# Performance work log

Hardware: AMD Instinct MI355X
Metric: run time of the kernel (lower is better)

## Reference

```python
import jax, jax.numpy as jnp
import numpy as np

B, S, D = 2, 2048, 1024
H, DK, DV = 16, 64, 64
MASKED = True


def setup_inputs() -> dict:
    key = jax.random.key(0)
    ks = jax.random.split(key, 12)
    s = 0.02
    inp = {
        "Q": jax.random.normal(ks[0], (B, S, D), jnp.float32),
        "K": jax.random.normal(ks[1], (B, S, D), jnp.float32),
        "V": jax.random.normal(ks[2], (B, S, D), jnp.float32),
        "pad_mask": jax.random.randint(ks[3], (B, S), 0, 2, jnp.int32),
        "Wq": jax.random.normal(ks[4], (D, H * DK), jnp.float32) * s,
        "bq": jnp.zeros((H * DK,), jnp.float32),
        "Wk": jax.random.normal(ks[5], (D, H * DK), jnp.float32) * s,
        "bk": jnp.zeros((H * DK,), jnp.float32),
        "Wv": jax.random.normal(ks[6], (D, H * DV), jnp.float32) * s,
        "bv": jnp.zeros((H * DV,), jnp.float32),
        "Wo": jax.random.normal(ks[7], (H * DV, D), jnp.float32) * s,
        "bo": jnp.zeros((D,), jnp.float32),
    }
    return inp


def _split(x):
    # [B,S,H*d] -> [B,H,S,d]
    b, s, _ = x.shape
    return x.reshape(b, s, H, -1).transpose(0, 2, 1, 3)


def reference(Q, K, V, pad_mask, Wq, bq, Wk, bk, Wv, bv, Wo, bo):
    q = _split(Q @ Wq + bq)  # [B,H,S,DK]
    k = _split(K @ Wk + bk)  # [B,H,S,DK]
    v = _split(V @ Wv + bv)  # [B,H,S,DV]

    scores = jnp.einsum("bhqd,bhkd->bhqk", q, k) / np.sqrt(DK)
    mask = pad_mask[:, None, None, :].astype(jnp.float32)  # [B,1,1,S]
    if MASKED:
        causal = jnp.triu(jnp.ones((S, S), jnp.float32), k=1)[None, None]
        mask = ((mask + causal) > 0).astype(jnp.float32)
    scores = scores - 1e9 * mask

    attn = jax.nn.softmax(scores, axis=-1)
    out = jnp.einsum("bhqk,bhkd->bhqd", attn, v)  # [B,H,S,DV]
    out = out.transpose(0, 2, 1, 3).reshape(B, S, H * DV)
    return out @ Wo + bo
```

## Files before the change

kernel.cpp:

```cpp
#include <hip/hip_runtime.h>

typedef unsigned short u16;
typedef unsigned int u32;

typedef __attribute__((ext_vector_type(8))) short bfrag;
typedef __attribute__((ext_vector_type(4))) float f32x4;
typedef __attribute__((ext_vector_type(8))) u16 u16x8;
typedef __attribute__((ext_vector_type(4))) u16 u16x4;

constexpr int S = 2048;
constexpr int HN = 16;
constexpr float QSCALE = 0.18033688011112042f;
constexpr float NBIG   = -1.442695e9f;

__device__ __forceinline__ u16 f2b(float f) {
  u32 u = __builtin_bit_cast(u32, f);
  return (u16)((u + 0x7FFFu + ((u >> 16) & 1u)) >> 16);
}
__device__ __forceinline__ float b2f(u16 v) {
  u32 u = (u32)v << 16;
  return __builtin_bit_cast(float, u);
}
__device__ __forceinline__ u32 cvtpk(float lo, float hi) {
  u32 d;
  asm("v_cvt_pk_bf16_f32 %0, %1, %2" : "=v"(d) : "v"(lo), "v"(hi));
  return d;
}
__device__ __forceinline__ float fexp2(float x) { return __builtin_amdgcn_exp2f(x); }

__device__ __forceinline__ f32x4 mfma16(bfrag a, bfrag b, f32x4 c) {
  return __builtin_amdgcn_mfma_f32_16x16x32_bf16(a, b, c, 0, 0, 0);
}

__device__ __forceinline__ void gload_lds16(const void* g, void* l) {
  __builtin_amdgcn_global_load_lds(
      (const __attribute__((address_space(1))) u32*)g,
      (__attribute__((address_space(3))) u32*)l, 16, 0, 0);
}

__global__ __launch_bounds__(256) void wtrans_kernel(
    const float* __restrict__ W0, const float* __restrict__ W1,
    const float* __restrict__ W2, const float* __restrict__ W3,
    u16* __restrict__ ws)
{
  const float* W = blockIdx.z == 0 ? W0 : blockIdx.z == 1 ? W1 : blockIdx.z == 2 ? W2 : W3;
  const float sc = blockIdx.z == 0 ? QSCALE : 1.0f;
  u16* WT = ws + (size_t)blockIdx.z * (1u << 20);
  __shared__ u16 tile[64 * 65];
  const int t = threadIdx.x;
  const int k0 = blockIdx.y * 64, n0 = blockIdx.x * 64;
#pragma unroll
  for (int i = 0; i < 4; ++i) {
    int idx = i * 256 + t;
    int r = idx >> 4, c4 = (idx & 15) * 4;
    float4 v = *(const float4*)&W[(size_t)(k0 + r) * 1024 + n0 + c4];
    tile[r * 65 + c4 + 0] = f2b(v.x * sc);
    tile[r * 65 + c4 + 1] = f2b(v.y * sc);
    tile[r * 65 + c4 + 2] = f2b(v.z * sc);
    tile[r * 65 + c4 + 3] = f2b(v.w * sc);
  }
  __syncthreads();
#pragma unroll
  for (int i = 0; i < 2; ++i) {
    int idx = i * 256 + t;
    int n = idx >> 3, k8 = (idx & 7) * 8;
    u16x8 o;
#pragma unroll
    for (int j = 0; j < 8; ++j) o[j] = tile[(k8 + j) * 65 + n];
    *(u16x8*)&WT[(size_t)(n0 + n) * 1024 + k0 + k8] = o;
  }
}

__global__ __launch_bounds__(256) void pscan_kernel(
    const int* __restrict__ pad, u16* __restrict__ idxc, u16* __restrict__ posT,
    int* __restrict__ eqt, float* __restrict__ colsumg)
{
  __shared__ int wtot[4];
  __shared__ int cntS;
  const int b = blockIdx.x;
  const int t = threadIdx.x, lane = t & 63, w = t >> 6;
  for (int i = t; i < 1024; i += 256) colsumg[b * 1024 + i] = 0.f;
  int4 p0 = *(const int4*)&pad[b * 2048 + t * 8];
  int4 p1 = *(const int4*)&pad[b * 2048 + t * 8 + 4];
  int u[8] = {p0.x == 0, p0.y == 0, p0.z == 0, p0.w == 0,
              p1.x == 0, p1.y == 0, p1.z == 0, p1.w == 0};
  int ps[8], run = 0;
#pragma unroll
  for (int j = 0; j < 8; ++j) { run += u[j]; ps[j] = run; }
  int sc = run;
#pragma unroll
  for (int o = 1; o < 64; o <<= 1) {
    int v = __shfl_up(sc, o);
    if (lane >= o) sc += v;
  }
  if (lane == 63) wtot[w] = sc;
  __syncthreads();
  int base = 0;
#pragma unroll
  for (int i = 0; i < 4; ++i) if (i < w) base += wtot[i];
  int excl = base + sc - run;
#pragma unroll
  for (int j = 0; j < 8; ++j)
    if (u[j]) idxc[b * 2048 + excl + ps[j] - 1] = (u16)(t * 8 + j);
  if ((t & 7) == 7) eqt[b * 32 + (t >> 3)] = base + sc;
  if (t == 255) cntS = base + sc;
  __syncthreads();
  const int cnt = cntS;
#pragma unroll
  for (int j = 0; j < 8; ++j) {
    int e = t * 8 + j;
    int pv = u[j] ? (excl + ps[j] - 1) : (cnt + e - excl - ps[j]);
    posT[b * 2048 + e] = (u16)pv;
  }
  for (int j = cnt + t; j < 2048; j += 256) idxc[b * 2048 + j] = 0x7FFF;
}

__global__ __launch_bounds__(256) void cvt_kernel(
    const float* __restrict__ A0, const float* __restrict__ A1,
    const float* __restrict__ A2, const u16* __restrict__ posT,
    u16* __restrict__ outbase)
{
  const int z = blockIdx.y;
  const float* A = z == 0 ? A0 : z == 1 ? A1 : A2;
  u16* dst = outbase + (size_t)z * (4u << 20);
  const int t = threadIdx.x;
  const int row = blockIdx.x * 2 + (t >> 7);
  const int col = (t & 127) * 8;
  int drow = row;
  if (z == 1) {
    int b = row >> 11;
    int p = posT[row];
    if (p >= 2048 - ((b == 0) ? 0 : 0)) {  }
    drow = b * 2048 + p;
  }
  const float* src = &A[(size_t)row * 1024 + col];
  float4 v0 = *(const float4*)src;
  float4 v1 = *(const float4*)(src + 4);
  union { u32 w[4]; u16x8 v; } o;
  o.w[0] = cvtpk(v0.x, v0.y); o.w[1] = cvtpk(v0.z, v0.w);
  o.w[2] = cvtpk(v1.x, v1.y); o.w[3] = cvtpk(v1.z, v1.w);
  *(u16x8*)&dst[(size_t)drow * 1024 + col] = o.v;
}

__global__ __launch_bounds__(256) void vgather_kernel(
    const u16* __restrict__ vb, const u16* __restrict__ idxc, u16* __restrict__ vTc)
{
  __shared__ u16 tile[64 * 65];
  const int ti = blockIdx.x, bh = blockIdx.y, b = bh >> 4;
  const int t = threadIdx.x;
#pragma unroll
  for (int i = 0; i < 2; ++i) {
    int idx = i * 256 + t;
    int r = idx >> 3, c8 = (idx & 7) * 8;
    int o = idxc[b * 2048 + ti * 64 + r];
    u16x8 in = {};
    if (o != 0x7FFF) in = *(const u16x8*)&vb[((size_t)bh * 2048 + o) * 64 + c8];
#pragma unroll
    for (int j = 0; j < 8; ++j) tile[r * 65 + c8 + j] = in[j];
  }
  __syncthreads();
#pragma unroll
  for (int i = 0; i < 2; ++i) {
    int idx = i * 256 + t;
    int dv = idx >> 3, s8 = (idx & 7) * 8;
    u16x8 o_;
#pragma unroll
    for (int j = 0; j < 8; ++j) o_[j] = tile[(s8 + j) * 65 + dv];
    int a = s8 >> 5, bb = (s8 >> 4) & 1, cc = (s8 >> 3) & 1;
    int s0l = a * 32 + cc * 16 + bb * 4;
    int x = (dv & 7) << 3;
    u16x4 lo = {o_[0], o_[1], o_[2], o_[3]};
    u16x4 hi = {o_[4], o_[5], o_[6], o_[7]};
    size_t rowbase = ((size_t)bh * 64 + dv) * S + ti * 64;
    *(u16x4*)&vTc[rowbase + (s0l ^ x)] = lo;
    *(u16x4*)&vTc[rowbase + ((s0l + 8) ^ x)] = hi;
  }
}

template <int CMODE>
__device__ __forceinline__ void gemm_core(
    u16* As, u16* Bs,
    const u16* __restrict__ A, const u16* __restrict__ Bt,
    const float* __restrict__ bias, void* __restrict__ Cout,
    int N, int K, int bn, int bm, float bscale,
    int kswz, float* __restrict__ csum)
{
  const int tid = threadIdx.x;
  const int wid = tid >> 6, lane = tid & 63;
  const int g = lane >> 4, c = lane & 15;
  const int wr = wid >> 1, wc = wid & 1;

  f32x4 acc[4][2] = {};

  const int nkt = K >> 6;
  for (int kt = 0; kt < nkt; ++kt) {
#pragma unroll
    for (int p = 0; p < 4; ++p) {
      int off = (p * 4 + wid) * 1024 + (lane << 4);
      int row = off >> 7, colb = off & 127;
      gload_lds16(&A[(size_t)(bm * 128 + row) * K + kt * 64 +
                     ((colb ^ ((row & 7) << 4)) >> 1)],
                  (char*)As + (p * 4 + wid) * 1024);
    }
#pragma unroll
    for (int p = 0; p < 2; ++p) {
      int off = (p * 4 + wid) * 1024 + (lane << 4);
      int row = off >> 7, colb = off & 127;
      gload_lds16(&Bt[(size_t)(bn * 64 + row) * K + kt * 64 +
                      ((colb ^ ((row & 7) << 4)) >> 1)],
                  (char*)Bs + (p * 4 + wid) * 1024);
    }
    __syncthreads();

#pragma unroll
    for (int ks = 0; ks < 2; ++ks) {
      bfrag af[4], bf[2];
#pragma unroll
      for (int mi = 0; mi < 4; ++mi) {
        int row = wr * 64 + mi * 16 + c;
        af[mi] = *(const bfrag*)&As[row * 64 + ((ks * 32 + g * 8) ^ ((row & 7) << 3))];
      }
#pragma unroll
      for (int ni = 0; ni < 2; ++ni) {
        int row = wc * 32 + ni * 16 + c;
        bf[ni] = *(const bfrag*)&Bs[row * 64 + ((ks * 32 + g * 8) ^ ((row & 7) << 3))];
      }
#pragma unroll
      for (int mi = 0; mi < 4; ++mi)
#pragma unroll
        for (int ni = 0; ni < 2; ++ni)
          acc[mi][ni] = mfma16(af[mi], bf[ni], acc[mi][ni]);
    }
    __syncthreads();
  }

  float colacc[2] = {0.f, 0.f};
#pragma unroll
  for (int mi = 0; mi < 4; ++mi) {
#pragma unroll
    for (int ni = 0; ni < 2; ++ni) {
#pragma unroll
      for (int j = 0; j < 4; ++j) {
        int rowg = bm * 128 + wr * 64 + mi * 16 + g * 4 + j;
        int colg = bn * 64 + wc * 32 + ni * 16 + c;
        float val = fmaf(bias[colg], bscale, acc[mi][ni][j]);
        if (CMODE == 0) {
          int b = rowg >> 11, s = rowg & (S - 1);
          int h = colg >> 6, d = colg & 63;
          if (kswz) d ^= (s & 7) << 3;
          if (csum) colacc[ni] += val;
          ((u16*)Cout)[((size_t)((b * HN + h) * S + s)) * 64 + d] = f2b(val);
        } else {
          ((float*)Cout)[(size_t)rowg * N + colg] = val;
        }
      }
    }
  }
  if (CMODE == 0 && csum) {
#pragma unroll
    for (int ni = 0; ni < 2; ++ni) {
      float s_ = colacc[ni];
      s_ += __shfl_xor(s_, 16);
      s_ += __shfl_xor(s_, 32);
      if (lane < 16) {
        int colg = bn * 64 + wc * 32 + ni * 16 + c;
        int b = (bm * 128) >> 11;
        atomicAdd(&csum[b * 1024 + colg], s_);
      }
    }
  }
}

__global__ __launch_bounds__(256) void qkv_gemm(
    const u16* __restrict__ Abase, const u16* __restrict__ WTbase,
    const float* __restrict__ b0, const float* __restrict__ b1, const float* __restrict__ b2,
    u16* __restrict__ qb, u16* __restrict__ kc, u16* __restrict__ vb,
    const int* __restrict__ eqt, float* __restrict__ colsumg)
{
  __shared__ __align__(16) u16 As[128 * 64];
  __shared__ __align__(16) u16 Bs[64 * 64];
  const int bid = blockIdx.x;
  const int l = (bid & 7) * 192 + (bid >> 3);
  const int z = l >> 9, rem = l & 511, bm = rem >> 4, bn = rem & 15;
  if (z == 1) {
    int b_ = (bm * 128) >> 11;
    int cnt_ = eqt[b_ * 32 + 31];
    if (((bm * 128) & 2047) >= cnt_) return;
  }
  const u16* A = Abase + (size_t)z * (4u << 20);
  const u16* Bt = WTbase + (size_t)z * (1u << 20);
  const float* bias = z == 0 ? b0 : z == 1 ? b1 : b2;
  u16* C = z == 0 ? qb : z == 1 ? kc : vb;
  gemm_core<0>(As, Bs, A, Bt, bias, C, 1024, 1024, bn, bm,
               z == 0 ? QSCALE : 1.0f,
               z == 1 ? 1 : 0,
               z == 2 ? colsumg : nullptr);
}

__global__ __launch_bounds__(256) void out_gemm(
    const u16* __restrict__ Av, const u16* __restrict__ Bt,
    const float* __restrict__ bias, void* __restrict__ Cout)
{
  __shared__ __align__(16) u16 As[128 * 64];
  __shared__ __align__(16) u16 Bs[64 * 64];
  const int bid = blockIdx.x;
  const int l = (bid & 7) * 64 + (bid >> 3);
  const int bm = l >> 4, bn = l & 15;
  gemm_core<1>(As, Bs, Av, Bt, bias, Cout, 1024, 1024, bn, bm, 1.0f,
               0, nullptr);
}

__global__ __launch_bounds__(256) void attn_kernel(
    const u16* __restrict__ q, const u16* __restrict__ kc,
    const u16* __restrict__ vTc, const u16* __restrict__ idxc,
    const int* __restrict__ eqt, const float* __restrict__ colsumg,
    u16* __restrict__ ao)
{
  __shared__ __align__(16) u16 Ks[2][64 * 64];
  __shared__ __align__(16) u16 Vs[2][64 * 64];

  const int tid = threadIdx.x;
  const int wid = tid >> 6, lane = tid & 63;
  const int g = lane >> 4, c = lane & 15;
  const int i = blockIdx.x;
  const int qt = 31 - (i >> 5);
  const int bh = i & 31;
  const int b = bh >> 4, h = bh & 15;

  const u16* idxb = idxc + b * 2048;
  const int ecnt = eqt[b * 32 + qt];
  const int nt = (ecnt + 63) >> 6;
  const int fz = idxb[0];
  const int qbasew = qt * 64 + wid * 16;
  const int qrow = qbasew + c;

  bfrag qf[2];
#pragma unroll
  for (int ks = 0; ks < 2; ++ks)
    qf[ks] = *(const bfrag*)&q[((size_t)bh * S + qrow) * 64 + ks * 32 + g * 8];

  float m = -3.0e38f, lsum = 0.f;
  f32x4 acc[4] = {};

  const size_t kbase = (size_t)bh * S * 64;
  const size_t vbase = (size_t)bh * 64 * S;
  const int sb = wid * 2048 + (lane << 4);
  const int sb2 = sb + 1024;

#define STAGE(buf, t)                                                              \
  do {                                                                             \
    gload_lds16(&kc[kbase + (size_t)(t) * 4096 + (sb >> 1)],                       \
                (char*)Ks[buf] + wid * 2048);                                      \
    gload_lds16(&kc[kbase + (size_t)(t) * 4096 + (sb2 >> 1)],                      \
                (char*)Ks[buf] + wid * 2048 + 1024);                               \
    gload_lds16(&vTc[vbase + (size_t)(sb >> 7) * S + (t) * 64 + ((sb & 127) >> 1)],\
                (char*)Vs[buf] + wid * 2048);                                      \
    gload_lds16(&vTc[vbase + (size_t)(sb2 >> 7) * S + (t) * 64 + ((sb2 & 127) >> 1)],\
                (char*)Vs[buf] + wid * 2048 + 1024);                               \
  } while (0)

  if (nt > 0) {
    STAGE(0, 0);
    __syncthreads();

    int cur = 0;
    for (int t = 0; t < nt; ++t) {
      if (t + 1 < nt) { STAGE(cur ^ 1, t + 1); }

      f32x4 sc[4] = {};
      __builtin_amdgcn_s_setprio(1);
#pragma unroll
      for (int ks = 0; ks < 2; ++ks)
#pragma unroll
        for (int nf = 0; nf < 4; ++nf) {
          int row = nf * 16 + c;
          bfrag kf = *(const bfrag*)&Ks[cur][row * 64 + ((ks * 32 + g * 8) ^ ((row & 7) << 3))];
          sc[nf] = mfma16(kf, qf[ks], sc[nf]);
        }
      __builtin_amdgcn_s_setprio(0);

      float sval[4][4];
#pragma unroll
      for (int nf = 0; nf < 4; ++nf)
#pragma unroll
        for (int r = 0; r < 4; ++r) sval[nf][r] = sc[nf][r];

      if ((int)idxb[t * 64 + 63] > qbasew) {
#pragma unroll
        for (int nf = 0; nf < 4; ++nf)
#pragma unroll
          for (int r = 0; r < 4; ++r) {
            int ov = idxb[t * 64 + nf * 16 + g * 4 + r];
            if (ov > qrow) sval[nf][r] = NBIG;
          }
      }

      float pm = sval[0][0];
#pragma unroll
      for (int nf = 0; nf < 4; ++nf)
#pragma unroll
        for (int r = 0; r < 4; ++r) pm = fmaxf(pm, sval[nf][r]);
      pm = fmaxf(pm, __shfl_xor(pm, 16));
      pm = fmaxf(pm, __shfl_xor(pm, 32));
      if (!__all(pm - m <= 11.5416f)) {
        float mn = fmaxf(m, pm);
        float fac = fexp2(m - mn);
        lsum *= fac;
#pragma unroll
        for (int nf = 0; nf < 4; ++nf)
#pragma unroll
          for (int j = 0; j < 4; ++j) acc[nf][j] *= fac;
        m = mn;
      }
      float p16v[4][4];
      float rs = 0.f;
#pragma unroll
      for (int nf = 0; nf < 4; ++nf)
#pragma unroll
        for (int r = 0; r < 4; ++r) {
          float pv = fexp2(sval[nf][r] - m);
          p16v[nf][r] = pv;
          rs += pv;
        }
      rs += __shfl_xor(rs, 16);
      rs += __shfl_xor(rs, 32);
      lsum += rs;

      bfrag pa[2];
#pragma unroll
      for (int ks = 0; ks < 2; ++ks) {
        union { u32 w[4]; bfrag f; } pu;
#pragma unroll
        for (int tt = 0; tt < 4; ++tt)
          pu.w[tt] = cvtpk(p16v[2 * ks + (tt >> 1)][2 * (tt & 1)],
                           p16v[2 * ks + (tt >> 1)][2 * (tt & 1) + 1]);
        pa[ks] = pu.f;
      }

      __builtin_amdgcn_s_setprio(1);
#pragma unroll
      for (int ks = 0; ks < 2; ++ks)
#pragma unroll
        for (int nf = 0; nf < 4; ++nf) {
          int row = nf * 16 + c;
          bfrag vf = *(const bfrag*)&Vs[cur][row * 64 + ((ks * 32 + g * 8) ^ ((row & 7) << 3))];
          acc[nf] = mfma16(vf, pa[ks], acc[nf]);
        }
      __builtin_amdgcn_s_setprio(0);

      __syncthreads();
      cur ^= 1;
    }
  }
#undef STAGE

  const float inv = 1.f / lsum;
#pragma unroll
  for (int nf = 0; nf < 4; ++nf) {
    u16x4 ov;
    if (qrow < fz) {
#pragma unroll
      for (int j = 0; j < 4; ++j)
        ov[j] = f2b(colsumg[bh * 64 + nf * 16 + g * 4 + j] * (1.f / 2048.f));
    } else {
#pragma unroll
      for (int j = 0; j < 4; ++j) ov[j] = f2b(acc[nf][j] * inv);
    }
    *(u16x4*)&ao[((size_t)b * S + qrow) * 1024 + h * 64 + nf * 16 + g * 4] = ov;
  }
}

extern "C" void kernel_launch(void* const* d_in, const int* in_sizes, int n_in,
                              void* d_out, int out_size, void* d_ws, size_t ws_size,
                              hipStream_t stream)
{
  const float* Q  = (const float*)d_in[0];
  const float* Kk = (const float*)d_in[1];
  const float* V  = (const float*)d_in[2];
  const int* pad  = (const int*)d_in[3];
  const float* Wq = (const float*)d_in[4];
  const float* bq = (const float*)d_in[5];
  const float* Wk = (const float*)d_in[6];
  const float* bk = (const float*)d_in[7];
  const float* Wv = (const float*)d_in[8];
  const float* bv = (const float*)d_in[9];
  const float* Wo = (const float*)d_in[10];
  const float* bo = (const float*)d_in[11];

  u16* ws  = (u16*)d_ws;
  u16* WoT = ws + 3 * (size_t)(1u << 20);
  u16* qb  = ws + 4 * (size_t)(1u << 20);
  u16* kc  = ws + 8 * (size_t)(1u << 20);
  u16* vb  = ws + 12 * (size_t)(1u << 20);
  u16* vTc = ws + 16 * (size_t)(1u << 20);
  u16* Abf = ws + 20 * (size_t)(1u << 20);
  u16* tab = ws + 32 * (size_t)(1u << 20);
  float* colsumg = (float*)tab;
  u16* idxc = tab + 4096;
  u16* posT = tab + 8192;
  int* eqt  = (int*)(tab + 12288);
  u16* ao   = vb;

  wtrans_kernel<<<dim3(16, 16, 4), 256, 0, stream>>>(Wq, Wk, Wv, Wo, ws);
  pscan_kernel<<<2, 256, 0, stream>>>(pad, idxc, posT, eqt, colsumg);
  cvt_kernel<<<dim3(2048, 3), 256, 0, stream>>>(Q, Kk, V, posT, Abf);
  qkv_gemm<<<1536, 256, 0, stream>>>(Abf, ws, bq, bk, bv, qb, kc, vb, eqt, colsumg);
  vgather_kernel<<<dim3(32, 32), 256, 0, stream>>>(vb, idxc, vTc);
  attn_kernel<<<1024, 256, 0, stream>>>(qb, kc, vTc, idxc, eqt, colsumg, ao);
  out_gemm<<<512, 256, 0, stream>>>(ao, WoT, bo, d_out);
}
```

Baseline: 105.3 us.

## Process 128 query rows per attention block and fuse pad scan into weight transpose

The attention kernel now has each wave handle two 16-row query sub-tiles, so every K/V tile staged in LDS is reused across 128 query rows and the grid halves to 512 blocks. This raises MFMA work per shared-memory load but doubles accumulator registers and may lower occupancy or leave fewer blocks for load balancing. Separately, the pad-mask prefix-scan kernel is merged into the weight-transpose launch as an extra z-slice, removing one kernel launch. Most of the blocks in that extra slice exit immediately.

```diff
diff --git a/kernel.cpp b/kernel.cpp
--- a/kernel.cpp
+++ b/kernel.cpp
@@ -41,13 +41,59 @@
 __global__ __launch_bounds__(256) void wtrans_kernel(
     const float* __restrict__ W0, const float* __restrict__ W1,
     const float* __restrict__ W2, const float* __restrict__ W3,
-    u16* __restrict__ ws)
-{
+    u16* __restrict__ ws,
+    const int* __restrict__ pad, u16* __restrict__ idxc, u16* __restrict__ posT,
+    int* __restrict__ eqt, float* __restrict__ colsumg)
+{
+  __shared__ u16 tile[64 * 65];
+  const int t = threadIdx.x;
+
+  if (blockIdx.z == 4) {
+    if (blockIdx.y != 0 || blockIdx.x >= 2) return;
+    int* wtot = (int*)tile;
+    int* cntS = (int*)tile + 4;
+    const int b = blockIdx.x;
+    const int lane = t & 63, w = t >> 6;
+    for (int i = t; i < 1024; i += 256) colsumg[b * 1024 + i] = 0.f;
+    int4 p0 = *(const int4*)&pad[b * 2048 + t * 8];
+    int4 p1 = *(const int4*)&pad[b * 2048 + t * 8 + 4];
+    int u[8] = {p0.x == 0, p0.y == 0, p0.z == 0, p0.w == 0,
+                p1.x == 0, p1.y == 0, p1.z == 0, p1.w == 0};
+    int ps[8], run = 0;
+#pragma unroll
+    for (int j = 0; j < 8; ++j) { run += u[j]; ps[j] = run; }
+    int sc = run;
+#pragma unroll
+    for (int o = 1; o < 64; o <<= 1) {
+      int v = __shfl_up(sc, o);
+      if (lane >= o) sc += v;
+    }
+    if (lane == 63) wtot[w] = sc;
+    __syncthreads();
+    int base = 0;
+#pragma unroll
+    for (int i = 0; i < 4; ++i) if (i < w) base += wtot[i];
+    int excl = base + sc - run;
+#pragma unroll
+    for (int j = 0; j < 8; ++j)
+      if (u[j]) idxc[b * 2048 + excl + ps[j] - 1] = (u16)(t * 8 + j);
+    if ((t & 7) == 7) eqt[b * 32 + (t >> 3)] = base + sc;
+    if (t == 255) *cntS = base + sc;
+    __syncthreads();
+    const int cnt = *cntS;
+#pragma unroll
+    for (int j = 0; j < 8; ++j) {
+      int e = t * 8 + j;
+      int pv = u[j] ? (excl + ps[j] - 1) : (cnt + e - excl - ps[j]);
+      posT[b * 2048 + e] = (u16)pv;
+    }
+    for (int j = cnt + t; j < 2048; j += 256) idxc[b * 2048 + j] = 0x7FFF;
+    return;
+  }
+
   const float* W = blockIdx.z == 0 ? W0 : blockIdx.z == 1 ? W1 : blockIdx.z == 2 ? W2 : W3;
   const float sc = blockIdx.z == 0 ? QSCALE : 1.0f;
   u16* WT = ws + (size_t)blockIdx.z * (1u << 20);
-  __shared__ u16 tile[64 * 65];
-  const int t = threadIdx.x;
   const int k0 = blockIdx.y * 64, n0 = blockIdx.x * 64;
 #pragma unroll
   for (int i = 0; i < 4; ++i) {
@@ -69,50 +115,6 @@
     for (int j = 0; j < 8; ++j) o[j] = tile[(k8 + j) * 65 + n];
     *(u16x8*)&WT[(size_t)(n0 + n) * 1024 + k0 + k8] = o;
   }
-}
-
-__global__ __launch_bounds__(256) void pscan_kernel(
-    const int* __restrict__ pad, u16* __restrict__ idxc, u16* __restrict__ posT,
-    int* __restrict__ eqt, float* __restrict__ colsumg)
-{
-  __shared__ int wtot[4];
-  __shared__ int cntS;
-  const int b = blockIdx.x;
-  const int t = threadIdx.x, lane = t & 63, w = t >> 6;
-  for (int i = t; i < 1024; i += 256) colsumg[b * 1024 + i] = 0.f;
-  int4 p0 = *(const int4*)&pad[b * 2048 + t * 8];
-  int4 p1 = *(const int4*)&pad[b * 2048 + t * 8 + 4];
-  int u[8] = {p0.x == 0, p0.y == 0, p0.z == 0, p0.w == 0,
-              p1.x == 0, p1.y == 0, p1.z == 0, p1.w == 0};
-  int ps[8], run = 0;
-#pragma unroll
-  for (int j = 0; j < 8; ++j) { run += u[j]; ps[j] = run; }
-  int sc = run;
-#pragma unroll
-  for (int o = 1; o < 64; o <<= 1) {
-    int v = __shfl_up(sc, o);
-    if (lane >= o) sc += v;
-  }
-  if (lane == 63) wtot[w] = sc;
-  __syncthreads();
-  int base = 0;
-#pragma unroll
-  for (int i = 0; i < 4; ++i) if (i < w) base += wtot[i];
-  int excl = base + sc - run;
-#pragma unroll
-  for (int j = 0; j < 8; ++j)
-    if (u[j]) idxc[b * 2048 + excl + ps[j] - 1] = (u16)(t * 8 + j);
-  if ((t & 7) == 7) eqt[b * 32 + (t >> 3)] = base + sc;
-  if (t == 255) cntS = base + sc;
-  __syncthreads();
-  const int cnt = cntS;
-#pragma unroll
-  for (int j = 0; j < 8; ++j) {
-    int e = t * 8 + j;
-    int pv = u[j] ? (excl + ps[j] - 1) : (cnt + e - excl - ps[j]);
-    posT[b * 2048 + e] = (u16)pv;
-  }
-  for (int j = cnt + t; j < 2048; j += 256) idxc[b * 2048 + j] = 0x7FFF;
 }
 
 __global__ __launch_bounds__(256) void cvt_kernel(
@@ -129,9 +131,7 @@
   int drow = row;
   if (z == 1) {
     int b = row >> 11;
-    int p = posT[row];
-    if (p >= 2048 - ((b == 0) ? 0 : 0)) {  }
-    drow = b * 2048 + p;
+    drow = b * 2048 + posT[row];
   }
   const float* src = &A[(size_t)row * 1024 + col];
   float4 v0 = *(const float4*)src;
@@ -323,24 +323,26 @@
   const int wid = tid >> 6, lane = tid & 63;
   const int g = lane >> 4, c = lane & 15;
   const int i = blockIdx.x;
-  const int qt = 31 - (i >> 5);
+  const int qt = 15 - (i >> 5);
   const int bh = i & 31;
   const int b = bh >> 4, h = bh & 15;
 
   const u16* idxb = idxc + b * 2048;
-  const int ecnt = eqt[b * 32 + qt];
+  const int ecnt = eqt[b * 32 + 2 * qt + 1];
   const int nt = (ecnt + 63) >> 6;
   const int fz = idxb[0];
-  const int qbasew = qt * 64 + wid * 16;
-  const int qrow = qbasew + c;
-
-  bfrag qf[2];
-#pragma unroll
-  for (int ks = 0; ks < 2; ++ks)
-    qf[ks] = *(const bfrag*)&q[((size_t)bh * S + qrow) * 64 + ks * 32 + g * 8];
-
-  float m = -3.0e38f, lsum = 0.f;
-  f32x4 acc[4] = {};
+
+  bfrag qf[2][2];
+#pragma unroll
+  for (int u = 0; u < 2; ++u)
+#pragma unroll
+    for (int ks = 0; ks < 2; ++ks)
+      qf[u][ks] = *(const bfrag*)&q[((size_t)bh * S + qt * 128 + wid * 32 + u * 16 + c) * 64 +
+                                    ks * 32 + g * 8];
+
+  float m[2] = {-3.0e38f, -3.0e38f};
+  float lsum[2] = {0.f, 0.f};
+  f32x4 acc[2][4] = {};
 
   const size_t kbase = (size_t)bh * S * 64;
   const size_t vbase = (size_t)bh * 64 * S;
@@ -367,7 +369,7 @@
     for (int t = 0; t < nt; ++t) {
       if (t + 1 < nt) { STAGE(cur ^ 1, t + 1); }
 
-      f32x4 sc[4] = {};
+      f32x4 sc[2][4] = {};
       __builtin_amdgcn_s_setprio(1);
 #pragma unroll
       for (int ks = 0; ks < 2; ++ks)
@@ -375,66 +377,71 @@
         for (int nf = 0; nf < 4; ++nf) {
           int row = nf * 16 + c;
           bfrag kf = *(const bfrag*)&Ks[cur][row * 64 + ((ks * 32 + g * 8) ^ ((row & 7) << 3))];
-          sc[nf] = mfma16(kf, qf[ks], sc[nf]);
+#pragma unroll
+          for (int u = 0; u < 2; ++u)
+            sc[u][nf] = mfma16(kf, qf[u][ks], sc[u][nf]);
         }
       __builtin_amdgcn_s_setprio(0);
 
-      float sval[4][4];
-#pragma unroll
-      for (int nf = 0; nf < 4; ++nf)
-#pragma unroll
-        for (int r = 0; r < 4; ++r) sval[nf][r] = sc[nf][r];
-
-      if ((int)idxb[t * 64 + 63] > qbasew) {
+      const int lastidx = (int)idxb[t * 64 + 63];
+      bfrag pa[2][2];
+#pragma unroll
+      for (int u = 0; u < 2; ++u) {
+        const int qb_u = qt * 128 + wid * 32 + u * 16;
+        const int qrow = qb_u + c;
+        float sval[4][4];
 #pragma unroll
         for (int nf = 0; nf < 4; ++nf)
 #pragma unroll
+          for (int r = 0; r < 4; ++r) sval[nf][r] = sc[u][nf][r];
+        if (lastidx > qb_u) {
+#pragma unroll
+          for (int nf = 0; nf < 4; ++nf)
+#pragma unroll
+            for (int r = 0; r < 4; ++r) {
+              int ov = idxb[t * 64 + nf * 16 + g * 4 + r];
+              if (ov > qrow) sval[nf][r] = NBIG;
+            }
+        }
+        float pm = sval[0][0];
+#pragma unroll
+        for (int nf = 0; nf < 4; ++nf)
+#pragma unroll
+          for (int r = 0; r < 4; ++r) pm = fmaxf(pm, sval[nf][r]);
+        pm = fmaxf(pm, __shfl_xor(pm, 16));
+        pm = fmaxf(pm, __shfl_xor(pm, 32));
+        if (!__all(pm - m[u] <= 11.5416f)) {
+          float mn = fmaxf(m[u], pm);
+          float fac = fexp2(m[u] - mn);
+          lsum[u] *= fac;
+#pragma unroll
+          for (int nf = 0; nf < 4; ++nf)
+#pragma unroll
+            for (int j = 0; j < 4; ++j) acc[u][nf][j] *= fac;
+          m[u] = mn;
+        }
+        float p16v[4][4];
+        float rs = 0.f;
+#pragma unroll
+        for (int nf = 0; nf < 4; ++nf)
+#pragma unroll
           for (int r = 0; r < 4; ++r) {
-            int ov = idxb[t * 64 + nf * 16 + g * 4 + r];
-            if (ov > qrow) sval[nf][r] = NBIG;
+            float pv = fexp2(sval[nf][r] - m[u]);
+            p16v[nf][r] = pv;
+            rs += pv;
           }
-      }
-
-      float pm = sval[0][0];
-#pragma unroll
-      for (int nf = 0; nf < 4; ++nf)
-#pragma unroll
-        for (int r = 0; r < 4; ++r) pm = fmaxf(pm, sval[nf][r]);
-      pm = fmaxf(pm, __shfl_xor(pm, 16));
-      pm = fmaxf(pm, __shfl_xor(pm, 32));
-      if (!__all(pm - m <= 11.5416f)) {
-        float mn = fmaxf(m, pm);
-        float fac = fexp2(m - mn);
-        lsum *= fac;
-#pragma unroll
-        for (int nf = 0; nf < 4; ++nf)
-#pragma unroll
-          for (int j = 0; j < 4; ++j) acc[nf][j] *= fac;
-        m = mn;
-      }
-      float p16v[4][4];
-      float rs = 0.f;
-#pragma unroll
-      for (int nf = 0; nf < 4; ++nf)
-#pragma unroll
-        for (int r = 0; r < 4; ++r) {
-          float pv = fexp2(sval[nf][r] - m);
-          p16v[nf][r] = pv;
-          rs += pv;
+        rs += __shfl_xor(rs, 16);
+        rs += __shfl_xor(rs, 32);
+        lsum[u] += rs;
+#pragma unroll
+        for (int ks = 0; ks < 2; ++ks) {
+          union { u32 w[4]; bfrag f; } pu;
+#pragma unroll
+          for (int tt = 0; tt < 4; ++tt)
+            pu.w[tt] = cvtpk(p16v[2 * ks + (tt >> 1)][2 * (tt & 1)],
+                             p16v[2 * ks + (tt >> 1)][2 * (tt & 1) + 1]);
+          pa[u][ks] = pu.f;
         }
-      rs += __shfl_xor(rs, 16);
-      rs += __shfl_xor(rs, 32);
-      lsum += rs;
-
-      bfrag pa[2];
-#pragma unroll
-      for (int ks = 0; ks < 2; ++ks) {
-        union { u32 w[4]; bfrag f; } pu;
-#pragma unroll
-        for (int tt = 0; tt < 4; ++tt)
-          pu.w[tt] = cvtpk(p16v[2 * ks + (tt >> 1)][2 * (tt & 1)],
-                           p16v[2 * ks + (tt >> 1)][2 * (tt & 1) + 1]);
-        pa[ks] = pu.f;
       }
 
       __builtin_amdgcn_s_setprio(1);
@@ -444,7 +451,9 @@
         for (int nf = 0; nf < 4; ++nf) {
           int row = nf * 16 + c;
           bfrag vf = *(const bfrag*)&Vs[cur][row * 64 + ((ks * 32 + g * 8) ^ ((row & 7) << 3))];
-          acc[nf] = mfma16(vf, pa[ks], acc[nf]);
+#pragma unroll
+          for (int u = 0; u < 2; ++u)
+            acc[u][nf] = mfma16(vf, pa[u][ks], acc[u][nf]);
         }
       __builtin_amdgcn_s_setprio(0);
 
@@ -454,19 +463,23 @@
   }
 #undef STAGE
 
-  const float inv = 1.f / lsum;
-#pragma unroll
-  for (int nf = 0; nf < 4; ++nf) {
-    u16x4 ov;
-    if (qrow < fz) {
-#pragma unroll
-      for (int j = 0; j < 4; ++j)
-        ov[j] = f2b(colsumg[bh * 64 + nf * 16 + g * 4 + j] * (1.f / 2048.f));
-    } else {
-#pragma unroll
-      for (int j = 0; j < 4; ++j) ov[j] = f2b(acc[nf][j] * inv);
-    }
-    *(u16x4*)&ao[((size_t)b * S + qrow) * 1024 + h * 64 + nf * 16 + g * 4] = ov;
+#pragma unroll
+  for (int u = 0; u < 2; ++u) {
+    const float inv = 1.f / lsum[u];
+    const int qrow = qt * 128 + wid * 32 + u * 16 + c;
+#pragma unroll
+    for (int nf = 0; nf < 4; ++nf) {
+      u16x4 ov;
+      if (qrow < fz) {
+#pragma unroll
+        for (int j = 0; j < 4; ++j)
+          ov[j] = f2b(colsumg[bh * 64 + nf * 16 + g * 4 + j] * (1.f / 2048.f));
+      } else {
+#pragma unroll
+        for (int j = 0; j < 4; ++j) ov[j] = f2b(acc[u][nf][j] * inv);
+      }
+      *(u16x4*)&ao[((size_t)b * S + qrow) * 1024 + h * 64 + nf * 16 + g * 4] = ov;
+    }
   }
 }
 
@@ -501,11 +514,11 @@
   int* eqt  = (int*)(tab + 12288);
   u16* ao   = vb;
 
-  wtrans_kernel<<<dim3(16, 16, 4), 256, 0, stream>>>(Wq, Wk, Wv, Wo, ws);
-  pscan_kernel<<<2, 256, 0, stream>>>(pad, idxc, posT, eqt, colsumg);
+  wtrans_kernel<<<dim3(16, 16, 5), 256, 0, stream>>>(Wq, Wk, Wv, Wo, ws,
+                                                     pad, idxc, posT, eqt, colsumg);
   cvt_kernel<<<dim3(2048, 3), 256, 0, stream>>>(Q, Kk, V, posT, Abf);
   qkv_gemm<<<1536, 256, 0, stream>>>(Abf, ws, bq, bk, bv, qb, kc, vb, eqt, colsumg);
   vgather_kernel<<<dim3(32, 32), 256, 0, stream>>>(vb, idxc, vTc);
-  attn_kernel<<<1024, 256, 0, stream>>>(qb, kc, vTc, idxc, eqt, colsumg, ao);
+  attn_kernel<<<512, 256, 0, stream>>>(qb, kc, vTc, idxc, eqt, colsumg, ao);
   out_gemm<<<512, 256, 0, stream>>>(ao, WoT, bo, d_out);
 }
```

Result: slower. 113.8 us (+8.1%).
